# Kernel optimization log

Measured on AMD Instinct MI355X. Metric: run time of the kernel, lower is better.

## Reference

```python
import jax, jax.numpy as jnp
import numpy as np

N = 50000  # nodes


def gcn_layer(x, src, dst, W, b):
    """DGL GraphConv with norm='both': D_in^{-1/2} A^T D_out^{-1/2} x W + b."""
    E = src.shape[0]
    ones = jnp.ones((E,), dtype=x.dtype)
    deg_out = jax.ops.segment_sum(ones, src, num_segments=N)  # out-degree of src nodes
    deg_in = jax.ops.segment_sum(ones, dst, num_segments=N)   # in-degree of dst nodes
    norm_src = jax.lax.rsqrt(jnp.maximum(deg_out, 1.0))
    norm_dst = jax.lax.rsqrt(jnp.maximum(deg_in, 1.0))
    h = x * norm_src[:, None]
    agg = jax.ops.segment_sum(h[src], dst, num_segments=N)  # [N, in_dim]
    return (agg @ W) * norm_dst[:, None] + b


def encoder(feat, src, dst, W1, b1, W2, b2):
    h = jax.nn.relu(gcn_layer(feat, src, dst, W1, b1))
    h = jax.nn.relu(gcn_layer(h, src, dst, W2, b2))
    return h


def proj(h, fc1_W, fc1_b, fc2_W, fc2_b):
    z = jax.nn.elu(h @ fc1_W + fc1_b)
    return z @ fc2_W + fc2_b


def setup_inputs() -> dict:
    key = jax.random.key(0)
    ks = jax.random.split(key, 12)
    in_dim, hid, out_dim, E = 128, 128, 128, 800000
    inp = {
        "feat1": jax.random.normal(ks[0], (N, in_dim), dtype=jnp.float32),
        "feat2": jax.random.normal(ks[1], (N, in_dim), dtype=jnp.float32),
        "edge_index1": jax.random.randint(ks[2], (2, E), 0, N),
        "edge_index2": jax.random.randint(ks[3], (2, E), 0, N),
        # GraphConv weights: in_dim -> 2*hid -> hid
        "conv1_W": jax.random.normal(ks[4], (in_dim, 2 * hid), dtype=jnp.float32) * 0.05,
        "conv1_b": jnp.zeros((2 * hid,), dtype=jnp.float32),
        "conv2_W": jax.random.normal(ks[5], (2 * hid, hid), dtype=jnp.float32) * 0.05,
        "conv2_b": jnp.zeros((hid,), dtype=jnp.float32),
        # MLP proj: fc1 hid->out, fc2 out->hid
        "fc1_W": jax.random.normal(ks[6], (hid, out_dim), dtype=jnp.float32) * 0.05,
        "fc1_b": jnp.zeros((out_dim,), dtype=jnp.float32),
        "fc2_W": jax.random.normal(ks[7], (out_dim, hid), dtype=jnp.float32) * 0.05,
        "fc2_b": jnp.zeros((hid,), dtype=jnp.float32),
    }
    return inp


def reference(feat1, feat2, edge_index1, edge_index2,
              conv1_W, conv1_b, conv2_W, conv2_b,
              fc1_W, fc1_b, fc2_W, fc2_b):
    h1 = encoder(feat1, edge_index1[0], edge_index1[1], conv1_W, conv1_b, conv2_W, conv2_b)
    h2 = encoder(feat2, edge_index2[0], edge_index2[1], conv1_W, conv1_b, conv2_W, conv2_b)
    z1 = proj(h1, fc1_W, fc1_b, fc2_W, fc2_b)
    z2 = proj(h2, fc1_W, fc1_b, fc2_W, fc2_b)
    return (z1, z2)
```

## Files before the change

### kernel.cpp

```cpp
#include <hip/hip_runtime.h>
#include <math.h>

#define NDIM 128
#define H2   256
#define MAXG 2
#define TPE  8192
#define NBKMAX 512

typedef __attribute__((ext_vector_type(8))) short bf16x8;
typedef __attribute__((ext_vector_type(4))) float f32x4;

__device__ __forceinline__ unsigned short f2bf(float f) {
    unsigned int u = __float_as_uint(f);
    u += 0x7fffu + ((u >> 16) & 1u);
    return (unsigned short)(u >> 16);
}
__device__ __forceinline__ float bf2f(unsigned short h) {
    return __uint_as_float(((unsigned int)h) << 16);
}
__device__ __forceinline__ void split2(float f, unsigned short& h, unsigned short& l) {
    h = f2bf(f);
    l = f2bf(f - bf2f(h));
}

struct BinArgs {
    const int* src[MAXG]; const int* dst[MAXG];
    int* histD[MAXG]; int* histS[MAXG];
    int* totD[MAXG];  int* baseD[MAXG];
    int* totS[MAXG];  int* baseS[MAXG];
    unsigned int* pairs[MAXG];
    unsigned short* srcS[MAXG];
    int E[MAXG]; int NBK; int NT; int n;
};

__global__ __launch_bounds__(256) void binA(BinArgs a) {
    __shared__ int cntD[NBKMAX], cntS[NBKMAX];
    int g = blockIdx.y, t = blockIdx.x, tid = threadIdx.x;
    for (int b = tid; b < NBKMAX; b += 256) { cntD[b] = 0; cntS[b] = 0; }
    __syncthreads();
    int E = a.E[g];
    int base = t * TPE;
#pragma unroll
    for (int k = 0; k < TPE / 256; ++k) {
        int e = base + k * 256 + tid;
        if (e < E) {
            atomicAdd(&cntD[a.dst[g][e] >> 7], 1);
            atomicAdd(&cntS[a.src[g][e] >> 7], 1);
        }
    }
    __syncthreads();
    for (int b = tid; b < a.NBK; b += 256) {
        a.histD[g][t * a.NBK + b] = cntD[b];
        a.histS[g][t * a.NBK + b] = cntS[b];
    }
}

__global__ __launch_bounds__(512) void binB(BinArgs a) {
    int g = blockIdx.y, side = blockIdx.z;
    int* hist = side ? a.histS[g] : a.histD[g];
    int* tot  = side ? a.totS[g]  : a.totD[g];
    int* base = side ? a.baseS[g] : a.baseD[g];
    __shared__ int s[512];
    int b = threadIdx.x;
    int v = 0;
    if (b < a.NBK)
        for (int t = 0; t < a.NT; ++t) v += hist[t * a.NBK + b];
    s[b] = v;
    __syncthreads();
    for (int off = 1; off < 512; off <<= 1) {
        int u = (b >= off) ? s[b - off] : 0;
        __syncthreads();
        s[b] += u;
        __syncthreads();
    }
    int excl = s[b] - v;
    if (b < a.NBK) {
        tot[b] = v;
        base[b] = excl;
        int run = excl;
        for (int t = 0; t < a.NT; ++t) {
            int h = hist[t * a.NBK + b];
            hist[t * a.NBK + b] = run;
            run += h;
        }
    }
}

__global__ __launch_bounds__(256) void binC(BinArgs a) {
    __shared__ int offD[NBKMAX], offS[NBKMAX];
    int g = blockIdx.y, t = blockIdx.x, tid = threadIdx.x;
    for (int b = tid; b < a.NBK; b += 256) {
        offD[b] = a.histD[g][t * a.NBK + b];
        offS[b] = a.histS[g][t * a.NBK + b];
    }
    __syncthreads();
    int E = a.E[g];
    int base = t * TPE;
    unsigned int* pairs = a.pairs[g];
    unsigned short* ss = a.srcS[g];
#pragma unroll
    for (int k = 0; k < TPE / 256; ++k) {
        int e = base + k * 256 + tid;
        if (e < E) {
            int s = a.src[g][e], d = a.dst[g][e];
            int pos = atomicAdd(&offD[d >> 7], 1);
            pairs[pos] = ((unsigned int)(d & 127) << 16) | (unsigned int)s;
            int posS = atomicAdd(&offS[s >> 7], 1);
            ss[posS] = (unsigned short)s;
        }
    }
}

struct FinArgs {
    const unsigned int* pairs[MAXG];
    const unsigned short* srcS[MAXG];
    const int* totD[MAXG]; const int* baseD[MAXG];
    const int* totS[MAXG]; const int* baseS[MAXG];
    int* row_ptr[MAXG]; int* row_end[MAXG];
    unsigned short* edge_srt[MAXG];
    float* ns[MAXG]; float* nd[MAXG];
    int n;
};

__global__ __launch_bounds__(256) void finalize(FinArgs a) {
    __shared__ int cnt[128], hist[128], scn[128], cur[128];
    int g = blockIdx.y, bkt = blockIdx.x, tid = threadIdx.x;
    if (tid < 128) { cnt[tid] = 0; hist[tid] = 0; }
    __syncthreads();
    {
        int base = a.baseS[g][bkt], tot = a.totS[g][bkt];
        const unsigned short* ss = a.srcS[g];
        for (int i = tid; i < tot; i += 256)
            atomicAdd(&cnt[ss[base + i] & 127], 1);
    }
    int cntE = a.totD[g][bkt], base = a.baseD[g][bkt];
    const unsigned int* pp = a.pairs[g] + base;
    for (int i = tid; i < cntE; i += 256)
        atomicAdd(&hist[pp[i] >> 16], 1);
    __syncthreads();
    if (tid < 128) {
        int node = bkt * 128 + tid;
        if (node < a.n) {
            int c = cnt[tid];
            a.ns[g][node] = rsqrtf((float)(c > 1 ? c : 1));
        }
        scn[tid] = hist[tid];
    }
    __syncthreads();
    for (int off = 1; off < 128; off <<= 1) {
        int v = (tid < 128 && tid >= off) ? scn[tid - off] : 0;
        __syncthreads();
        if (tid < 128) scn[tid] += v;
        __syncthreads();
    }
    if (tid < 128) {
        int incl = scn[tid];
        int h = hist[tid];
        cur[tid] = incl - h;
        int node = bkt * 128 + tid;
        if (node < a.n) {
            a.row_ptr[g][node] = base + incl - h;
            a.row_end[g][node] = base + incl;
            a.nd[g][node] = rsqrtf((float)(h > 1 ? h : 1));
        }
    }
    __syncthreads();
    for (int i = tid; i < cntE; i += 256) {
        unsigned int p = pp[i];
        int pos = atomicAdd(&cur[p >> 16], 1);
        a.edge_srt[g][base + pos] = (unsigned short)(p & 0xFFFF);
    }
}

struct PreArgs { const float* X[MAXG]; const float* ns[MAXG]; float* Xs[MAXG]; int n; };

__global__ __launch_bounds__(256) void prescale(PreArgs a) {
    int g = blockIdx.y;
    int i = blockIdx.x * 256 + threadIdx.x;
    if (i >= a.n * 32) return;
    int row = i >> 5;
    float s = a.ns[g][row];
    float4 v = ((const float4*)a.X[g])[i];
    v.x *= s; v.y *= s; v.z *= s; v.w *= s;
    ((float4*)a.Xs[g])[i] = v;
}

struct GatherArgs {
    const float* X[MAXG];
    const int* row_ptr[MAXG]; const int* row_end[MAXG];
    const unsigned short* edge_src[MAXG];
    const float* nd[MAXG];
    unsigned short* outH[MAXG]; unsigned short* outL[MAXG];
    const float* bias; int use_nd; int n;
};

__global__ __launch_bounds__(256) void gather_split_b(GatherArgs a) {
    int g = blockIdx.y;
    int half = threadIdx.x >> 5;
    int lane = threadIdx.x & 31;
    int r = blockIdx.x * 8 + half;
    if (r >= a.n) return;
    int j = a.row_ptr[g][r];
    int end = a.row_end[g][r];
    const unsigned short* ep = a.edge_src[g];
    const float* X = a.X[g];
    int base = lane * 4;
    float4 acc = make_float4(0.f, 0.f, 0.f, 0.f);
    for (; j + 3 < end; j += 4) {
        int s0 = ep[j], s1 = ep[j + 1], s2 = ep[j + 2], s3 = ep[j + 3];
        float4 v0 = *(const float4*)(X + (size_t)s0 * NDIM + base);
        float4 v1 = *(const float4*)(X + (size_t)s1 * NDIM + base);
        float4 v2 = *(const float4*)(X + (size_t)s2 * NDIM + base);
        float4 v3 = *(const float4*)(X + (size_t)s3 * NDIM + base);
        acc.x += v0.x + v1.x + v2.x + v3.x;
        acc.y += v0.y + v1.y + v2.y + v3.y;
        acc.z += v0.z + v1.z + v2.z + v3.z;
        acc.w += v0.w + v1.w + v2.w + v3.w;
    }
    for (; j < end; ++j) {
        int s0 = ep[j];
        float4 v0 = *(const float4*)(X + (size_t)s0 * NDIM + base);
        acc.x += v0.x; acc.y += v0.y; acc.z += v0.z; acc.w += v0.w;
    }
    float v[4] = {acc.x, acc.y, acc.z, acc.w};
    if (a.use_nd) {
        float s = a.nd[g][r];
#pragma unroll
        for (int i = 0; i < 4; ++i)
            v[i] = fmaxf(v[i] * s + a.bias[base + i], 0.f);
    }
    unsigned short h[4], l[4];
#pragma unroll
    for (int i = 0; i < 4; ++i) split2(v[i], h[i], l[i]);
    *(ushort4*)(a.outH[g] + (size_t)r * NDIM + base) = make_ushort4(h[0], h[1], h[2], h[3]);
    *(ushort4*)(a.outL[g] + (size_t)r * NDIM + base) = make_ushort4(l[0], l[1], l[2], l[3]);
}

__global__ void wprep_all(const float* __restrict__ W1, const float* __restrict__ W2,
                          const float* __restrict__ F1, const float* __restrict__ F2,
                          unsigned short* __restrict__ W1h, unsigned short* __restrict__ W1l,
                          unsigned short* __restrict__ W2h, unsigned short* __restrict__ W2l,
                          unsigned short* __restrict__ F1h, unsigned short* __restrict__ F1l,
                          unsigned short* __restrict__ F2h, unsigned short* __restrict__ F2l) {
    int i = blockIdx.x * 256 + threadIdx.x;
    const float* Wsrc; unsigned short *Hd, *Ld; int K, Nc, idx;
    if (i < 32768)       { Wsrc = W1; Hd = W1h; Ld = W1l; K = 128; Nc = 256; idx = i; }
    else if (i < 65536)  { Wsrc = W2; Hd = W2h; Ld = W2l; K = 256; Nc = 128; idx = i - 32768; }
    else if (i < 81920)  { Wsrc = F1; Hd = F1h; Ld = F1l; K = 128; Nc = 128; idx = i - 65536; }
    else                 { Wsrc = F2; Hd = F2h; Ld = F2l; K = 128; Nc = 128; idx = i - 81920; }
    int k = idx / Nc, n = idx % Nc;
    unsigned short h, l;
    split2(Wsrc[idx], h, l);
    Hd[n * K + k] = h;
    Ld[n * K + k] = l;
}

struct GemmArgs {
    const unsigned short* Ah[MAXG]; const unsigned short* Al[MAXG];
    const unsigned short* Bh; const unsigned short* Bl;
    float* C[MAXG]; unsigned short* CH[MAXG]; unsigned short* CL[MAXG];
    const float* rsOut[MAXG]; const float* bOut;
    int M, K, Nc, act, has_rs, has_b, split_out;
};

__global__ __launch_bounds__(256) void mfma_gemm_b(GemmArgs a) {
    __shared__ __align__(16) unsigned short Ah[64 * 40];
    __shared__ __align__(16) unsigned short Al[64 * 40];
    __shared__ __align__(16) unsigned short Bh[128 * 40];
    __shared__ __align__(16) unsigned short Bl[128 * 40];

    int g = blockIdx.z;
    const unsigned short* Ah_g = a.Ah[g];
    const unsigned short* Al_g = a.Al[g];

    int tid  = threadIdx.x;
    int wave = tid >> 6, lane = tid & 63;
    int quad = lane >> 4, l16 = lane & 15;
    int rowBase = blockIdx.x * 64;
    int colBase = blockIdx.y * 128;
    int M = a.M, K = a.K, Nc = a.Nc;

    f32x4 acc[4][2] = {};

    int s_row   = tid >> 2;
    int s_chunk = (tid & 3) * 8;

    for (int k0 = 0; k0 < K; k0 += 32) {
        int gr = rowBase + s_row;
        uint4 va_h = make_uint4(0, 0, 0, 0), va_l = make_uint4(0, 0, 0, 0);
        if (gr < M) {
            va_h = *(const uint4*)(Ah_g + (size_t)gr * K + k0 + s_chunk);
            va_l = *(const uint4*)(Al_g + (size_t)gr * K + k0 + s_chunk);
        }
        *(uint4*)(Ah + s_row * 40 + s_chunk) = va_h;
        *(uint4*)(Al + s_row * 40 + s_chunk) = va_l;
#pragma unroll
        for (int c = tid; c < 512; c += 256) {
            int bn = c >> 2, bc = (c & 3) * 8;
            uint4 vb_h = *(const uint4*)(a.Bh + (size_t)(colBase + bn) * K + k0 + bc);
            uint4 vb_l = *(const uint4*)(a.Bl + (size_t)(colBase + bn) * K + k0 + bc);
            *(uint4*)(Bh + bn * 40 + bc) = vb_h;
            *(uint4*)(Bl + bn * 40 + bc) = vb_l;
        }
        __syncthreads();

        bf16x8 af[4], alf[4], bhf[2], blf[2];
#pragma unroll
        for (int i = 0; i < 4; ++i) {
            af[i]  = *(const bf16x8*)(Ah + (i * 16 + l16) * 40 + quad * 8);
            alf[i] = *(const bf16x8*)(Al + (i * 16 + l16) * 40 + quad * 8);
        }
#pragma unroll
        for (int j = 0; j < 2; ++j) {
            bhf[j] = *(const bf16x8*)(Bh + (wave * 32 + j * 16 + l16) * 40 + quad * 8);
            blf[j] = *(const bf16x8*)(Bl + (wave * 32 + j * 16 + l16) * 40 + quad * 8);
        }
#pragma unroll
        for (int i = 0; i < 4; ++i)
#pragma unroll
            for (int j = 0; j < 2; ++j) {
                acc[i][j] = __builtin_amdgcn_mfma_f32_16x16x32_bf16(af[i],  bhf[j], acc[i][j], 0, 0, 0);
                acc[i][j] = __builtin_amdgcn_mfma_f32_16x16x32_bf16(alf[i], bhf[j], acc[i][j], 0, 0, 0);
                acc[i][j] = __builtin_amdgcn_mfma_f32_16x16x32_bf16(af[i],  blf[j], acc[i][j], 0, 0, 0);
            }
        __syncthreads();
    }

#pragma unroll
    for (int i = 0; i < 4; ++i) {
#pragma unroll
        for (int r = 0; r < 4; ++r) {
            int row = rowBase + i * 16 + quad * 4 + r;
            if (row >= M) continue;
            float rs = a.has_rs ? a.rsOut[g][row] : 1.0f;
#pragma unroll
            for (int j = 0; j < 2; ++j) {
                int col = colBase + wave * 32 + j * 16 + l16;
                float v = acc[i][j][r] * rs;
                if (a.has_b) v += a.bOut[col];
                if (a.act == 1) v = fmaxf(v, 0.f);
                else if (a.act == 2) v = v > 0.f ? v : expm1f(v);
                if (a.split_out) {
                    unsigned short h, l;
                    split2(v, h, l);
                    a.CH[g][(size_t)row * Nc + col] = h;
                    a.CL[g][(size_t)row * Nc + col] = l;
                } else {
                    a.C[g][(size_t)row * Nc + col] = v;
                }
            }
        }
    }
}

extern "C" void kernel_launch(void* const* d_in, const int* in_sizes, int n_in,
                              void* d_out, int out_size, void* d_ws, size_t ws_size,
                              hipStream_t stream) {
    const float* feat[2] = {(const float*)d_in[0], (const float*)d_in[1]};
    const int*   ei[2]   = {(const int*)d_in[2], (const int*)d_in[3]};
    const float* W1   = (const float*)d_in[4];
    const float* b1   = (const float*)d_in[5];
    const float* W2   = (const float*)d_in[6];
    const float* b2   = (const float*)d_in[7];
    const float* fc1W = (const float*)d_in[8];
    const float* fc1b = (const float*)d_in[9];
    const float* fc2W = (const float*)d_in[10];
    const float* fc2b = (const float*)d_in[11];
    int N = in_sizes[0] / NDIM;
    float* out = (float*)d_out;

    int Emax = 0;
    for (int g = 0; g < 2; ++g) { int E = in_sizes[2 + g] / 2; if (E > Emax) Emax = E; }
    int NBK = (N + 127) / 128;
    int NT  = (Emax + TPE - 1) / TPE;

    char* p = (char*)d_ws;
    float* ns_[2]; float* nd_[2];
    for (int i = 0; i < 2; ++i) { ns_[i] = (float*)p; p += (size_t)N * 4; }
    for (int i = 0; i < 2; ++i) { nd_[i] = (float*)p; p += (size_t)N * 4; }
    int* rp_[2]; int* re_[2]; unsigned short* esrt_[2];
    for (int i = 0; i < 2; ++i) { rp_[i] = (int*)p; p += (size_t)N * 4; }
    for (int i = 0; i < 2; ++i) { re_[i] = (int*)p; p += (size_t)N * 4; }
    for (int i = 0; i < 2; ++i) { esrt_[i] = (unsigned short*)p; p += (size_t)Emax * 2; }
    unsigned short* R1[2]; unsigned short* R2[2];
    for (int i = 0; i < 2; ++i) { R1[i] = (unsigned short*)p; p += (size_t)N * NDIM * 2 * 2; }
    for (int i = 0; i < 2; ++i) { R2[i] = (unsigned short*)p; p += (size_t)N * H2 * 2 * 2; }
    unsigned short* W1th = (unsigned short*)p; p += (size_t)NDIM * H2 * 2;
    unsigned short* W1tl = (unsigned short*)p; p += (size_t)NDIM * H2 * 2;
    unsigned short* W2th = (unsigned short*)p; p += (size_t)H2 * NDIM * 2;
    unsigned short* W2tl = (unsigned short*)p; p += (size_t)H2 * NDIM * 2;
    unsigned short* f1th = (unsigned short*)p; p += (size_t)NDIM * NDIM * 2;
    unsigned short* f1tl = (unsigned short*)p; p += (size_t)NDIM * NDIM * 2;
    unsigned short* f2th = (unsigned short*)p; p += (size_t)NDIM * NDIM * 2;
    unsigned short* f2tl = (unsigned short*)p; p += (size_t)NDIM * NDIM * 2;
    int* tb = (int*)p; p += (size_t)2 * 4 * NBK * 4;

    int* histD_[2]; int* histS_[2]; unsigned int* pairs_[2]; unsigned short* srcS_[2];
    float* Xs_[2];
    for (int i = 0; i < 2; ++i) {
        histD_[i] = (int*)R2[i];
        histS_[i] = (int*)R2[i] + (size_t)NT * NBK;
        pairs_[i] = (unsigned int*)((char*)R2[i] + (1 << 20));
        srcS_[i]  = (unsigned short*)R1[i];
        Xs_[i]    = (float*)R2[i];
    }

    BinArgs ba = {};
    ba.NBK = NBK; ba.NT = NT; ba.n = N;
    for (int i = 0; i < 2; ++i) {
        int E = in_sizes[2 + i] / 2;
        ba.src[i] = ei[i]; ba.dst[i] = ei[i] + E; ba.E[i] = E;
        ba.histD[i] = histD_[i]; ba.histS[i] = histS_[i];
        ba.totD[i]  = tb + (size_t)i * 4 * NBK;
        ba.baseD[i] = tb + (size_t)i * 4 * NBK + NBK;
        ba.totS[i]  = tb + (size_t)i * 4 * NBK + 2 * NBK;
        ba.baseS[i] = tb + (size_t)i * 4 * NBK + 3 * NBK;
        ba.pairs[i] = pairs_[i]; ba.srcS[i] = srcS_[i];
    }

    wprep_all<<<384, 256, 0, stream>>>(W1, W2, fc1W, fc2W,
                                       W1th, W1tl, W2th, W2tl, f1th, f1tl, f2th, f2tl);
    binA<<<dim3(NT, 2), 256, 0, stream>>>(ba);
    binB<<<dim3(1, 2, 2), 512, 0, stream>>>(ba);
    binC<<<dim3(NT, 2), 256, 0, stream>>>(ba);

    FinArgs fa = {};
    fa.n = N;
    for (int i = 0; i < 2; ++i) {
        fa.pairs[i] = pairs_[i]; fa.srcS[i] = srcS_[i];
        fa.totD[i] = ba.totD[i]; fa.baseD[i] = ba.baseD[i];
        fa.totS[i] = ba.totS[i]; fa.baseS[i] = ba.baseS[i];
        fa.row_ptr[i] = rp_[i]; fa.row_end[i] = re_[i];
        fa.edge_srt[i] = esrt_[i];
        fa.ns[i] = ns_[i]; fa.nd[i] = nd_[i];
    }
    finalize<<<dim3(NBK, 2), 256, 0, stream>>>(fa);

    PreArgs pa = {};
    pa.n = N;
    for (int i = 0; i < 2; ++i) { pa.X[i] = feat[i]; pa.ns[i] = ns_[i]; pa.Xs[i] = Xs_[i]; }
    prescale<<<dim3((N * 32 + 255) / 256, 2), 256, 0, stream>>>(pa);

    unsigned short *A1h[2], *A1l[2], *X1h[2], *X1l[2], *Gh[2], *Gl[2], *Zh[2], *Zl[2];
    float* T[2];
    for (int i = 0; i < 2; ++i) {
        A1h[i] = R1[i]; A1l[i] = R1[i] + (size_t)N * NDIM;
        T[i]   = (float*)R1[i];
        Zh[i]  = R1[i]; Zl[i]  = R1[i] + (size_t)N * NDIM;
        X1h[i] = R2[i]; X1l[i] = R2[i] + (size_t)N * H2;
        Gh[i]  = R2[i]; Gl[i]  = R2[i] + (size_t)N * NDIM;
    }

    int ggrid = (N + 7) / 8;
    int mgrid = (N + 63) / 64;

    GatherArgs ga = {};
    ga.n = N; ga.use_nd = 0; ga.bias = b2;
    for (int i = 0; i < 2; ++i) {
        ga.X[i] = Xs_[i];
        ga.row_ptr[i] = rp_[i]; ga.row_end[i] = re_[i]; ga.edge_src[i] = esrt_[i];
        ga.nd[i] = nd_[i];
        ga.outH[i] = A1h[i]; ga.outL[i] = A1l[i];
    }
    gather_split_b<<<dim3(ggrid, 2), 256, 0, stream>>>(ga);

    GemmArgs g1 = {};
    g1.Bh = W1th; g1.Bl = W1tl; g1.bOut = b1;
    g1.M = N; g1.K = NDIM; g1.Nc = H2; g1.act = 1; g1.has_rs = 1; g1.has_b = 1; g1.split_out = 1;
    for (int i = 0; i < 2; ++i) {
        g1.Ah[i] = A1h[i]; g1.Al[i] = A1l[i];
        g1.CH[i] = X1h[i]; g1.CL[i] = X1l[i]; g1.rsOut[i] = nd_[i];
    }
    mfma_gemm_b<<<dim3(mgrid, H2 / 128, 2), 256, 0, stream>>>(g1);

    GemmArgs g2 = {};
    g2.Bh = W2th; g2.Bl = W2tl;
    g2.M = N; g2.K = H2; g2.Nc = NDIM; g2.act = 0; g2.has_rs = 1; g2.has_b = 0; g2.split_out = 0;
    for (int i = 0; i < 2; ++i) {
        g2.Ah[i] = X1h[i]; g2.Al[i] = X1l[i]; g2.C[i] = T[i]; g2.rsOut[i] = ns_[i];
    }
    mfma_gemm_b<<<dim3(mgrid, 1, 2), 256, 0, stream>>>(g2);

    GatherArgs gb = ga;
    gb.use_nd = 1;
    for (int i = 0; i < 2; ++i) {
        gb.X[i] = T[i];
        gb.outH[i] = Gh[i]; gb.outL[i] = Gl[i];
    }
    gather_split_b<<<dim3(ggrid, 2), 256, 0, stream>>>(gb);

    GemmArgs g3 = {};
    g3.Bh = f1th; g3.Bl = f1tl; g3.bOut = fc1b;
    g3.M = N; g3.K = NDIM; g3.Nc = NDIM; g3.act = 2; g3.has_rs = 0; g3.has_b = 1; g3.split_out = 1;
    for (int i = 0; i < 2; ++i) {
        g3.Ah[i] = Gh[i]; g3.Al[i] = Gl[i];
        g3.CH[i] = Zh[i]; g3.CL[i] = Zl[i];
    }
    mfma_gemm_b<<<dim3(mgrid, 1, 2), 256, 0, stream>>>(g3);

    GemmArgs g4 = {};
    g4.Bh = f2th; g4.Bl = f2tl; g4.bOut = fc2b;
    g4.M = N; g4.K = NDIM; g4.Nc = NDIM; g4.act = 0; g4.has_rs = 0; g4.has_b = 1; g4.split_out = 0;
    for (int i = 0; i < 2; ++i) {
        g4.Ah[i] = Zh[i]; g4.Al[i] = Zl[i];
        g4.C[i] = out + (size_t)i * N * NDIM;
    }
    mfma_gemm_b<<<dim3(mgrid, 1, 2), 256, 0, stream>>>(g4);
}
```

Before: 631.7 us.

## Fuse source-norm prescale into gather and make GEMM load fragments directly from global

Drops the separate prescale kernel. The first gather now reads raw features and multiplies each gathered row by a per-source norm looked up during the gather, which saves a full read and write of the feature matrix. The MFMA GEMM is rewritten as a K-templated kernel that loads bf16 fragments straight from global memory instead of staging tiles in LDS, so its barriers go away. The cost is redundant global loads: the four waves reload the same A fragments, and B is reread per block through the cache. Out-of-range rows are clamped rather than zero-filled.

```diff
diff --git a/kernel.cpp b/kernel.cpp
--- a/kernel.cpp
+++ b/kernel.cpp
@@ -172,26 +172,14 @@
     }
 }
 
-struct PreArgs { const float* X[MAXG]; const float* ns[MAXG]; float* Xs[MAXG]; int n; };
-
-__global__ __launch_bounds__(256) void prescale(PreArgs a) {
-    int g = blockIdx.y;
-    int i = blockIdx.x * 256 + threadIdx.x;
-    if (i >= a.n * 32) return;
-    int row = i >> 5;
-    float s = a.ns[g][row];
-    float4 v = ((const float4*)a.X[g])[i];
-    v.x *= s; v.y *= s; v.z *= s; v.w *= s;
-    ((float4*)a.Xs[g])[i] = v;
-}
-
 struct GatherArgs {
     const float* X[MAXG];
     const int* row_ptr[MAXG]; const int* row_end[MAXG];
     const unsigned short* edge_src[MAXG];
     const float* nd[MAXG];
+    const float* sns[MAXG];
     unsigned short* outH[MAXG]; unsigned short* outL[MAXG];
-    const float* bias; int use_nd; int n;
+    const float* bias; int use_nd; int use_sns; int n;
 };
 
 __global__ __launch_bounds__(256) void gather_split_b(GatherArgs a) {
@@ -204,23 +192,46 @@
     int end = a.row_end[g][r];
     const unsigned short* ep = a.edge_src[g];
     const float* X = a.X[g];
+    const float* sns = a.sns[g];
     int base = lane * 4;
     float4 acc = make_float4(0.f, 0.f, 0.f, 0.f);
-    for (; j + 3 < end; j += 4) {
-        int s0 = ep[j], s1 = ep[j + 1], s2 = ep[j + 2], s3 = ep[j + 3];
-        float4 v0 = *(const float4*)(X + (size_t)s0 * NDIM + base);
-        float4 v1 = *(const float4*)(X + (size_t)s1 * NDIM + base);
-        float4 v2 = *(const float4*)(X + (size_t)s2 * NDIM + base);
-        float4 v3 = *(const float4*)(X + (size_t)s3 * NDIM + base);
-        acc.x += v0.x + v1.x + v2.x + v3.x;
-        acc.y += v0.y + v1.y + v2.y + v3.y;
-        acc.z += v0.z + v1.z + v2.z + v3.z;
-        acc.w += v0.w + v1.w + v2.w + v3.w;
-    }
-    for (; j < end; ++j) {
-        int s0 = ep[j];
-        float4 v0 = *(const float4*)(X + (size_t)s0 * NDIM + base);
-        acc.x += v0.x; acc.y += v0.y; acc.z += v0.z; acc.w += v0.w;
+    if (a.use_sns) {
+        for (; j + 3 < end; j += 4) {
+            int s0 = ep[j], s1 = ep[j + 1], s2 = ep[j + 2], s3 = ep[j + 3];
+            float n0 = sns[s0], n1 = sns[s1], n2 = sns[s2], n3 = sns[s3];
+            float4 v0 = *(const float4*)(X + (size_t)s0 * NDIM + base);
+            float4 v1 = *(const float4*)(X + (size_t)s1 * NDIM + base);
+            float4 v2 = *(const float4*)(X + (size_t)s2 * NDIM + base);
+            float4 v3 = *(const float4*)(X + (size_t)s3 * NDIM + base);
+            acc.x = fmaf(v0.x, n0, fmaf(v1.x, n1, fmaf(v2.x, n2, fmaf(v3.x, n3, acc.x))));
+            acc.y = fmaf(v0.y, n0, fmaf(v1.y, n1, fmaf(v2.y, n2, fmaf(v3.y, n3, acc.y))));
+            acc.z = fmaf(v0.z, n0, fmaf(v1.z, n1, fmaf(v2.z, n2, fmaf(v3.z, n3, acc.z))));
+            acc.w = fmaf(v0.w, n0, fmaf(v1.w, n1, fmaf(v2.w, n2, fmaf(v3.w, n3, acc.w))));
+        }
+        for (; j < end; ++j) {
+            int s0 = ep[j];
+            float n0 = sns[s0];
+            float4 v0 = *(const float4*)(X + (size_t)s0 * NDIM + base);
+            acc.x = fmaf(v0.x, n0, acc.x); acc.y = fmaf(v0.y, n0, acc.y);
+            acc.z = fmaf(v0.z, n0, acc.z); acc.w = fmaf(v0.w, n0, acc.w);
+        }
+    } else {
+        for (; j + 3 < end; j += 4) {
+            int s0 = ep[j], s1 = ep[j + 1], s2 = ep[j + 2], s3 = ep[j + 3];
+            float4 v0 = *(const float4*)(X + (size_t)s0 * NDIM + base);
+            float4 v1 = *(const float4*)(X + (size_t)s1 * NDIM + base);
+            float4 v2 = *(const float4*)(X + (size_t)s2 * NDIM + base);
+            float4 v3 = *(const float4*)(X + (size_t)s3 * NDIM + base);
+            acc.x += v0.x + v1.x + v2.x + v3.x;
+            acc.y += v0.y + v1.y + v2.y + v3.y;
+            acc.z += v0.z + v1.z + v2.z + v3.z;
+            acc.w += v0.w + v1.w + v2.w + v3.w;
+        }
+        for (; j < end; ++j) {
+            int s0 = ep[j];
+            float4 v0 = *(const float4*)(X + (size_t)s0 * NDIM + base);
+            acc.x += v0.x; acc.y += v0.y; acc.z += v0.z; acc.w += v0.w;
+        }
     }
     float v[4] = {acc.x, acc.y, acc.z, acc.w};
     if (a.use_nd) {
@@ -263,57 +274,48 @@
     int M, K, Nc, act, has_rs, has_b, split_out;
 };
 
-__global__ __launch_bounds__(256) void mfma_gemm_b(GemmArgs a) {
-    __shared__ __align__(16) unsigned short Ah[64 * 40];
-    __shared__ __align__(16) unsigned short Al[64 * 40];
-    __shared__ __align__(16) unsigned short Bh[128 * 40];
-    __shared__ __align__(16) unsigned short Bl[128 * 40];
-
+template <int KT>
+__global__ __launch_bounds__(256) void mfma_gemm_r(GemmArgs a) {
     int g = blockIdx.z;
-    const unsigned short* Ah_g = a.Ah[g];
-    const unsigned short* Al_g = a.Al[g];
+    const unsigned short* __restrict__ Ah_g = a.Ah[g];
+    const unsigned short* __restrict__ Al_g = a.Al[g];
+    const unsigned short* __restrict__ Bh = a.Bh;
+    const unsigned short* __restrict__ Bl = a.Bl;
 
     int tid  = threadIdx.x;
     int wave = tid >> 6, lane = tid & 63;
     int quad = lane >> 4, l16 = lane & 15;
     int rowBase = blockIdx.x * 64;
     int colBase = blockIdx.y * 128;
-    int M = a.M, K = a.K, Nc = a.Nc;
+    int M = a.M, Nc = a.Nc;
 
     f32x4 acc[4][2] = {};
 
-    int s_row   = tid >> 2;
-    int s_chunk = (tid & 3) * 8;
-
-    for (int k0 = 0; k0 < K; k0 += 32) {
-        int gr = rowBase + s_row;
-        uint4 va_h = make_uint4(0, 0, 0, 0), va_l = make_uint4(0, 0, 0, 0);
-        if (gr < M) {
-            va_h = *(const uint4*)(Ah_g + (size_t)gr * K + k0 + s_chunk);
-            va_l = *(const uint4*)(Al_g + (size_t)gr * K + k0 + s_chunk);
-        }
-        *(uint4*)(Ah + s_row * 40 + s_chunk) = va_h;
-        *(uint4*)(Al + s_row * 40 + s_chunk) = va_l;
-#pragma unroll
-        for (int c = tid; c < 512; c += 256) {
-            int bn = c >> 2, bc = (c & 3) * 8;
-            uint4 vb_h = *(const uint4*)(a.Bh + (size_t)(colBase + bn) * K + k0 + bc);
-            uint4 vb_l = *(const uint4*)(a.Bl + (size_t)(colBase + bn) * K + k0 + bc);
-            *(uint4*)(Bh + bn * 40 + bc) = vb_h;
-            *(uint4*)(Bl + bn * 40 + bc) = vb_l;
-        }
-        __syncthreads();
-
+    size_t aoff[4];
+#pragma unroll
+    for (int i = 0; i < 4; ++i) {
+        int row = rowBase + i * 16 + l16;
+        if (row > M - 1) row = M - 1;
+        aoff[i] = (size_t)row * KT + quad * 8;
+    }
+    size_t boff[2];
+#pragma unroll
+    for (int j = 0; j < 2; ++j)
+        boff[j] = (size_t)(colBase + wave * 32 + j * 16 + l16) * KT + quad * 8;
+
+#pragma unroll
+    for (int kt = 0; kt < KT / 32; ++kt) {
+        int k0 = kt * 32;
         bf16x8 af[4], alf[4], bhf[2], blf[2];
 #pragma unroll
         for (int i = 0; i < 4; ++i) {
-            af[i]  = *(const bf16x8*)(Ah + (i * 16 + l16) * 40 + quad * 8);
-            alf[i] = *(const bf16x8*)(Al + (i * 16 + l16) * 40 + quad * 8);
+            af[i]  = *(const bf16x8*)(Ah_g + aoff[i] + k0);
+            alf[i] = *(const bf16x8*)(Al_g + aoff[i] + k0);
         }
 #pragma unroll
         for (int j = 0; j < 2; ++j) {
-            bhf[j] = *(const bf16x8*)(Bh + (wave * 32 + j * 16 + l16) * 40 + quad * 8);
-            blf[j] = *(const bf16x8*)(Bl + (wave * 32 + j * 16 + l16) * 40 + quad * 8);
+            bhf[j] = *(const bf16x8*)(Bh + boff[j] + k0);
+            blf[j] = *(const bf16x8*)(Bl + boff[j] + k0);
         }
 #pragma unroll
         for (int i = 0; i < 4; ++i)
@@ -323,7 +325,6 @@
                 acc[i][j] = __builtin_amdgcn_mfma_f32_16x16x32_bf16(alf[i], bhf[j], acc[i][j], 0, 0, 0);
                 acc[i][j] = __builtin_amdgcn_mfma_f32_16x16x32_bf16(af[i],  blf[j], acc[i][j], 0, 0, 0);
             }
-        __syncthreads();
     }
 
 #pragma unroll
@@ -396,13 +397,11 @@
     int* tb = (int*)p; p += (size_t)2 * 4 * NBK * 4;
 
     int* histD_[2]; int* histS_[2]; unsigned int* pairs_[2]; unsigned short* srcS_[2];
-    float* Xs_[2];
     for (int i = 0; i < 2; ++i) {
         histD_[i] = (int*)R2[i];
         histS_[i] = (int*)R2[i] + (size_t)NT * NBK;
         pairs_[i] = (unsigned int*)((char*)R2[i] + (1 << 20));
         srcS_[i]  = (unsigned short*)R1[i];
-        Xs_[i]    = (float*)R2[i];
     }
 
     BinArgs ba = {};
@@ -436,11 +435,6 @@
     }
     finalize<<<dim3(NBK, 2), 256, 0, stream>>>(fa);
 
-    PreArgs pa = {};
-    pa.n = N;
-    for (int i = 0; i < 2; ++i) { pa.X[i] = feat[i]; pa.ns[i] = ns_[i]; pa.Xs[i] = Xs_[i]; }
-    prescale<<<dim3((N * 32 + 255) / 256, 2), 256, 0, stream>>>(pa);
-
     unsigned short *A1h[2], *A1l[2], *X1h[2], *X1l[2], *Gh[2], *Gl[2], *Zh[2], *Zl[2];
     float* T[2];
     for (int i = 0; i < 2; ++i) {
@@ -455,11 +449,11 @@
     int mgrid = (N + 63) / 64;
 
     GatherArgs ga = {};
-    ga.n = N; ga.use_nd = 0; ga.bias = b2;
-    for (int i = 0; i < 2; ++i) {
-        ga.X[i] = Xs_[i];
+    ga.n = N; ga.use_nd = 0; ga.use_sns = 1; ga.bias = b2;
+    for (int i = 0; i < 2; ++i) {
+        ga.X[i] = feat[i];
         ga.row_ptr[i] = rp_[i]; ga.row_end[i] = re_[i]; ga.edge_src[i] = esrt_[i];
-        ga.nd[i] = nd_[i];
+        ga.nd[i] = nd_[i]; ga.sns[i] = ns_[i];
         ga.outH[i] = A1h[i]; ga.outL[i] = A1l[i];
     }
     gather_split_b<<<dim3(ggrid, 2), 256, 0, stream>>>(ga);
@@ -471,7 +465,7 @@
         g1.Ah[i] = A1h[i]; g1.Al[i] = A1l[i];
         g1.CH[i] = X1h[i]; g1.CL[i] = X1l[i]; g1.rsOut[i] = nd_[i];
     }
-    mfma_gemm_b<<<dim3(mgrid, H2 / 128, 2), 256, 0, stream>>>(g1);
+    mfma_gemm_r<128><<<dim3(mgrid, H2 / 128, 2), 256, 0, stream>>>(g1);
 
     GemmArgs g2 = {};
     g2.Bh = W2th; g2.Bl = W2tl;
@@ -479,10 +473,10 @@
     for (int i = 0; i < 2; ++i) {
         g2.Ah[i] = X1h[i]; g2.Al[i] = X1l[i]; g2.C[i] = T[i]; g2.rsOut[i] = ns_[i];
     }
-    mfma_gemm_b<<<dim3(mgrid, 1, 2), 256, 0, stream>>>(g2);
+    mfma_gemm_r<256><<<dim3(mgrid, 1, 2), 256, 0, stream>>>(g2);
 
     GatherArgs gb = ga;
-    gb.use_nd = 1;
+    gb.use_nd = 1; gb.use_sns = 0;
     for (int i = 0; i < 2; ++i) {
         gb.X[i] = T[i];
         gb.outH[i] = Gh[i]; gb.outL[i] = Gl[i];
@@ -496,7 +490,7 @@
         g3.Ah[i] = Gh[i]; g3.Al[i] = Gl[i];
         g3.CH[i] = Zh[i]; g3.CL[i] = Zl[i];
     }
-    mfma_gemm_b<<<dim3(mgrid, 1, 2), 256, 0, stream>>>(g3);
+    mfma_gemm_r<128><<<dim3(mgrid, 1, 2), 256, 0, stream>>>(g3);
 
     GemmArgs g4 = {};
     g4.Bh = f2th; g4.Bl = f2tl; g4.bOut = fc2b;
@@ -505,5 +499,5 @@
         g4.Ah[i] = Zh[i]; g4.Al[i] = Zl[i];
         g4.C[i] = out + (size_t)i * N * NDIM;
     }
-    mfma_gemm_b<<<dim3(mgrid, 1, 2), 256, 0, stream>>>(g4);
-}
+    mfma_gemm_r<128><<<dim3(mgrid, 1, 2), 256, 0, stream>>>(g4);
+}
```

After: 754.1 us. 19.4% more time.
